# Kernel optimization log

Hardware: AMD Instinct MI355X
Metric: run time of the kernel (lower is better)

## Reference

```python
import jax, jax.numpy as jnp
import numpy as np

B, H, S, D = 2, 16, 2048, 64


def setup_inputs() -> dict:
    key = jax.random.key(0)
    kq, kk, kv = jax.random.split(key, 3)
    q = jax.random.normal(kq, (B, H, S, D), dtype=jnp.float32)
    k = jax.random.normal(kk, (B, H, S, D), dtype=jnp.float32)
    v = jax.random.normal(kv, (B, H, S, D), dtype=jnp.float32)
    # True = attend (lower triangular); positions where mask == False get -1e9
    causal_mask = jnp.tril(jnp.ones((S, S), dtype=bool))
    return {"q": q, "k": k, "v": v, "causal_mask": causal_mask}


def reference(q, k, v, causal_mask):
    scale = q.shape[-1] ** 0.5
    # [b,h,s,d] @ [b,h,d,t] -> [b,h,s,t]
    pre_score = jnp.einsum("bhsd,bhtd->bhst", q, k) / scale
    pre_score = jnp.where(causal_mask, pre_score, jnp.float32(-1e9))
    # SafeSoftmax: stable softmax along last dim
    attn = jax.nn.softmax(pre_score, axis=-1)
    return jnp.einsum("bhst,bhtd->bhsd", attn, v)
```

## Files before the change

### kernel.cpp

```cpp
#include <hip/hip_runtime.h>


typedef __attribute__((ext_vector_type(8))) short short8;
typedef __attribute__((ext_vector_type(4))) short short4v;
typedef __attribute__((ext_vector_type(4))) float floatx4;
typedef __attribute__((ext_vector_type(4))) int intx4;

constexpr int S = 2048;
constexpr int D = 64;
constexpr int KSTR = 72;
constexpr int VSTR = 72;

__device__ inline short f2bf(float x){
    unsigned u = __builtin_bit_cast(unsigned, x);
    unsigned r = u + 0x7FFFu + ((u >> 16) & 1u);
    return (short)(r >> 16);
}
__device__ inline float fast_exp2(float x){ return __builtin_amdgcn_exp2f(x); }

__global__ __launch_bounds__(256, 2)
void fa_fwd_kernel(const float* __restrict__ Q, const float* __restrict__ K,
                   const float* __restrict__ V, float* __restrict__ Out)
{
    __shared__ short sK [2][64 * KSTR];
    __shared__ short sVt[2][64 * VSTR];

    const int tid  = threadIdx.x;
    const int wave = tid >> 6;
    const int lane = tid & 63;
    const int l16  = lane & 15;
    const int quad = lane >> 4;

    const unsigned ub = blockIdx.x;
    const int bh = (int)((ub & 7u) * 4u + (ub >> 7));
    const int qp = (int)((ub >> 3) & 15u);

    const float* Qb = Q + (size_t)bh * S * D;
    const float* Kb = K + (size_t)bh * S * D;
    const float* Vb = V + (size_t)bh * S * D;
    float* Ob = Out + (size_t)bh * S * D;

    const float qscale = 0.125f * 1.44269504f;

    const int kr = tid >> 2;
    const int kc = (tid & 3) * 16;
    const int vd0   = (tid & 15) * 4;
    const int vkey0 = (tid >> 4) * 4;
    const float* kSrc = Kb + (size_t)kr * D + kc;
    const float* vSrc = Vb + (size_t)vkey0 * D + vd0;

    floatx4 kpre[4], vpre[4];
#pragma unroll
    for (int i = 0; i < 4; ++i) kpre[i] = *(const floatx4*)(kSrc + i*4);
#pragma unroll
    for (int r = 0; r < 4; ++r) vpre[r] = *(const floatx4*)(vSrc + (size_t)r*D);

    int pb = 0;
#pragma unroll 1
    for (int seg = 0; seg < 2; ++seg){
        const int qt  = seg ? (31 - qp) : qp;
        const int nkb = qt + 1;
        const int r0  = qt * 64 + wave * 16;

        short8 qa[2];
        {
            const float* qptr = Qb + (size_t)(r0 + l16) * D + quad * 8;
#pragma unroll
            for (int kt = 0; kt < 2; ++kt){
                floatx4 f0 = *(const floatx4*)(qptr + kt*32);
                floatx4 f1 = *(const floatx4*)(qptr + kt*32 + 4);
                short8 v;
                v[0]=f2bf(f0.x*qscale); v[1]=f2bf(f0.y*qscale);
                v[2]=f2bf(f0.z*qscale); v[3]=f2bf(f0.w*qscale);
                v[4]=f2bf(f1.x*qscale); v[5]=f2bf(f1.y*qscale);
                v[6]=f2bf(f1.z*qscale); v[7]=f2bf(f1.w*qscale);
                qa[kt] = v;
            }
        }

        float mrow = -1e30f, lsum = 0.0f;
        floatx4 Oacc[4];
#pragma unroll
        for (int dt = 0; dt < 4; ++dt) Oacc[dt] = (floatx4){0.f,0.f,0.f,0.f};

#pragma unroll 1
        for (int kb = 0; kb < nkb; ++kb){
            const int n0 = kb * 64;

            {
                short8 w0, w1;
                w0[0]=f2bf(kpre[0].x); w0[1]=f2bf(kpre[0].y); w0[2]=f2bf(kpre[0].z); w0[3]=f2bf(kpre[0].w);
                w0[4]=f2bf(kpre[1].x); w0[5]=f2bf(kpre[1].y); w0[6]=f2bf(kpre[1].z); w0[7]=f2bf(kpre[1].w);
                w1[0]=f2bf(kpre[2].x); w1[1]=f2bf(kpre[2].y); w1[2]=f2bf(kpre[2].z); w1[3]=f2bf(kpre[2].w);
                w1[4]=f2bf(kpre[3].x); w1[5]=f2bf(kpre[3].y); w1[6]=f2bf(kpre[3].z); w1[7]=f2bf(kpre[3].w);
                *(short8*)&sK[pb][kr * KSTR + kc]     = w0;
                *(short8*)&sK[pb][kr * KSTR + kc + 8] = w1;
#pragma unroll
                for (int j = 0; j < 4; ++j){
                    short4v sj;
                    sj[0]=f2bf(vpre[0][j]); sj[1]=f2bf(vpre[1][j]);
                    sj[2]=f2bf(vpre[2][j]); sj[3]=f2bf(vpre[3][j]);
                    *(short4v*)&sVt[pb][(vd0 + j) * VSTR + vkey0] = sj;
                }
            }

            {
                const int n0n = (kb + 1 < nkb) ? (n0 + 64) : 0;
                const float* ks = kSrc + (size_t)n0n * D;
                const float* vs = vSrc + (size_t)n0n * D;
#pragma unroll
                for (int i = 0; i < 4; ++i) kpre[i] = *(const floatx4*)(ks + i*4);
#pragma unroll
                for (int r = 0; r < 4; ++r) vpre[r] = *(const floatx4*)(vs + (size_t)r*D);
            }

            __syncthreads();

            const int lastT = min(3, (r0 + 15 - n0) >> 4);

            float p[4][4];
#pragma unroll
            for (int t = 0; t < 4; ++t)
#pragma unroll
                for (int r = 0; r < 4; ++r) p[t][r] = 0.0f;

            float mx = -1e30f;
#pragma unroll
            for (int t = 0; t < 4; ++t){
                if (t > lastT) continue;
                const short8 kf0 = *(const short8*)&sK[pb][(t*16 + l16) * KSTR + quad*8];
                const short8 kf1 = *(const short8*)&sK[pb][(t*16 + l16) * KSTR + 32 + quad*8];
                floatx4 acc = (floatx4){0.f,0.f,0.f,0.f};
                acc = __builtin_amdgcn_mfma_f32_16x16x32_bf16(kf0, qa[0], acc, 0,0,0);
                acc = __builtin_amdgcn_mfma_f32_16x16x32_bf16(kf1, qa[1], acc, 0,0,0);
                if (n0 + t*16 + 15 > r0){
                    const int keyb = n0 + t*16 + quad*4;
                    const int qrow = r0 + l16;
#pragma unroll
                    for (int r = 0; r < 4; ++r)
                        acc[r] = (keyb + r <= qrow) ? acc[r] : -1e9f;
                }
#pragma unroll
                for (int r = 0; r < 4; ++r){ p[t][r] = acc[r]; mx = fmaxf(mx, acc[r]); }
            }
            mx = fmaxf(mx, __shfl_xor(mx, 16, 64));
            mx = fmaxf(mx, __shfl_xor(mx, 32, 64));

            const float mn = fmaxf(mrow, mx);
            const float al = fast_exp2(mrow - mn);
            mrow = mn;

            float rs = 0.0f;
#pragma unroll
            for (int t = 0; t < 4; ++t){
                if (t > lastT) continue;
#pragma unroll
                for (int r = 0; r < 4; ++r){
                    p[t][r] = fast_exp2(p[t][r] - mn);
                    rs += p[t][r];
                }
            }
            rs += __shfl_xor(rs, 16, 64);
            rs += __shfl_xor(rs, 32, 64);
            lsum = lsum * al + rs;
#pragma unroll
            for (int dt = 0; dt < 4; ++dt)
#pragma unroll
                for (int r = 0; r < 4; ++r) Oacc[dt][r] *= al;

            unsigned pk[4][2];
#pragma unroll
            for (int t = 0; t < 4; ++t)
#pragma unroll
                for (int h = 0; h < 2; ++h){
                    unsigned lo = __builtin_bit_cast(unsigned, p[t][2*h]);
                    unsigned hi = __builtin_bit_cast(unsigned, p[t][2*h+1]);
                    pk[t][h] = (lo >> 16) | (hi & 0xFFFF0000u);
                }

            const int addr_lo = (l16 + ((quad & 1) << 5)) << 2;
            const int addr_hi = addr_lo + 64;
            const bool hiQ = quad >= 2;
#pragma unroll
            for (int c = 0; c < 2; ++c){
                if (2*c > lastT) continue;
                const int ta = 2*c, tb = 2*c + 1;
                int a0 = __builtin_amdgcn_ds_bpermute(addr_lo, (int)pk[ta][0]);
                int b0 = __builtin_amdgcn_ds_bpermute(addr_lo, (int)pk[tb][0]);
                int a1 = __builtin_amdgcn_ds_bpermute(addr_lo, (int)pk[ta][1]);
                int b1 = __builtin_amdgcn_ds_bpermute(addr_lo, (int)pk[tb][1]);
                int a2 = __builtin_amdgcn_ds_bpermute(addr_hi, (int)pk[ta][0]);
                int b2 = __builtin_amdgcn_ds_bpermute(addr_hi, (int)pk[tb][0]);
                int a3 = __builtin_amdgcn_ds_bpermute(addr_hi, (int)pk[ta][1]);
                int b3 = __builtin_amdgcn_ds_bpermute(addr_hi, (int)pk[tb][1]);
                union { intx4 i4; short8 s8; } bf;
                bf.i4[0] = hiQ ? b0 : a0;
                bf.i4[1] = hiQ ? b1 : a1;
                bf.i4[2] = hiQ ? b2 : a2;
                bf.i4[3] = hiQ ? b3 : a3;
#pragma unroll
                for (int dt = 0; dt < 4; ++dt){
                    const short8 vf = *(const short8*)&sVt[pb][(dt*16 + l16) * VSTR + c*32 + quad*8];
                    Oacc[dt] = __builtin_amdgcn_mfma_f32_16x16x32_bf16(vf, bf.s8, Oacc[dt], 0,0,0);
                }
            }
            pb ^= 1;
        }

        const float inv = 1.0f / lsum;
        float* op = Ob + (size_t)(r0 + l16) * D + quad * 4;
#pragma unroll
        for (int dt = 0; dt < 4; ++dt){
            floatx4 o;
#pragma unroll
            for (int r = 0; r < 4; ++r) o[r] = Oacc[dt][r] * inv;
            *(floatx4*)(op + dt*16) = o;
        }
    }
}

extern "C" void kernel_launch(void* const* d_in, const int* in_sizes, int n_in,
                              void* d_out, int out_size, void* d_ws, size_t ws_size,
                              hipStream_t stream) {
    const float* q = (const float*)d_in[0];
    const float* k = (const float*)d_in[1];
    const float* v = (const float*)d_in[2];
    float* out = (float*)d_out;
    dim3 grid(512);
    dim3 block(256);
    hipLaunchKernelGGL(fa_fwd_kernel, grid, block, 0, stream, q, k, v, out);
}
```

Measured before the change: 154.6 us.

## Prepack K/V into bf16 MFMA fragment layout in workspace before attention

Adds a prepass kernel that converts K and V to bf16 and stores them in workspace already arranged in MFMA fragment order, with V transposed. The attention kernel then copies these fragments into shared memory with plain vector loads and stores, avoiding per-block conversion and the strided transpose. The grid also changes from 512 blocks each handling a paired light and heavy query tile to 1024 blocks of one tile each, launched heaviest-first, with 4 blocks per CU instead of 2. The cost is an extra kernel launch and a bf16 write and read pass through workspace; the original kernel is kept as a fallback when the workspace is too small.

After: 145.9 us. -5.6%, faster.

```diff
diff --git a/kernel.cpp b/kernel.cpp
--- a/kernel.cpp
+++ b/kernel.cpp
@@ -8,8 +8,9 @@
 
 constexpr int S = 2048;
 constexpr int D = 64;
-constexpr int KSTR = 72;
-constexpr int VSTR = 72;
+constexpr size_t TILE_SH = 8 * 64 * 8;
+constexpr size_t TENSOR_SH = 32ull * 32 * TILE_SH;
+constexpr size_t WS_NEEDED = 2 * TENSOR_SH * 2;
 
 __device__ inline short f2bf(float x){
     unsigned u = __builtin_bit_cast(unsigned, x);
@@ -18,12 +19,49 @@
 }
 __device__ inline float fast_exp2(float x){ return __builtin_amdgcn_exp2f(x); }
 
-__global__ __launch_bounds__(256, 2)
-void fa_fwd_kernel(const float* __restrict__ Q, const float* __restrict__ K,
-                   const float* __restrict__ V, float* __restrict__ Out)
+__global__ __launch_bounds__(256)
+void prepack_kernel(const float* __restrict__ K, const float* __restrict__ V,
+                    short* __restrict__ Kf, short* __restrict__ Vf)
 {
-    __shared__ short sK [2][64 * KSTR];
-    __shared__ short sVt[2][64 * VSTR];
+    const int blk = blockIdx.x;
+    const int bh = blk >> 5, kb = blk & 31;
+    const int tid = threadIdx.x;
+    const float* Kb = K + (size_t)bh * S * D + (size_t)kb * 64 * D;
+    const float* Vb = V + (size_t)bh * S * D + (size_t)kb * 64 * D;
+    short* Kfb = Kf + (size_t)(bh * 32 + kb) * TILE_SH;
+    short* Vfb = Vf + (size_t)(bh * 32 + kb) * TILE_SH;
+#pragma unroll
+    for (int h = 0; h < 2; ++h){
+        const int s = tid + h * 256;
+        const int f = s >> 6, lane = s & 63;
+        const int l16 = lane & 15, quad = lane >> 4;
+        {
+            const int t = f >> 1, kt = f & 1;
+            const float* src = Kb + (size_t)(t*16 + l16) * D + kt*32 + quad*8;
+            floatx4 a = *(const floatx4*)src;
+            floatx4 b = *(const floatx4*)(src + 4);
+            short8 v;
+            v[0]=f2bf(a.x); v[1]=f2bf(a.y); v[2]=f2bf(a.z); v[3]=f2bf(a.w);
+            v[4]=f2bf(b.x); v[5]=f2bf(b.y); v[6]=f2bf(b.z); v[7]=f2bf(b.w);
+            *(short8*)&Kfb[(size_t)s * 8] = v;
+        }
+        {
+            const int c = f >> 2, dt = f & 3;
+            const int d = dt*16 + l16, key0 = c*32 + quad*8;
+            short8 v;
+#pragma unroll
+            for (int j = 0; j < 8; ++j)
+                v[j] = f2bf(Vb[(size_t)(key0 + j) * D + d]);
+            *(short8*)&Vfb[(size_t)s * 8] = v;
+        }
+    }
+}
+
+__global__ __launch_bounds__(256, 4)
+void fa_fwd_kernel(const float* __restrict__ Q, const short* __restrict__ Kf,
+                   const short* __restrict__ Vf, float* __restrict__ Out)
+{
+    __shared__ short sF[2][16 * 512];
 
     const int tid  = threadIdx.x;
     const int wave = tid >> 6;
@@ -32,36 +70,202 @@
     const int quad = lane >> 4;
 
     const unsigned ub = blockIdx.x;
+    const int i  = (int)(ub >> 3);
+    const int bh = (int)(ub & 7u) * 4 + (i & 3);
+    const int qt = 31 - (i >> 2);
+    const int r0 = qt * 64 + wave * 16;
+    const int nkb = qt + 1;
+
+    const float* Qb = Q + (size_t)bh * S * D;
+    const short* Kfb = Kf + (size_t)bh * 32 * TILE_SH;
+    const short* Vfb = Vf + (size_t)bh * 32 * TILE_SH;
+    float* Ob = Out + (size_t)bh * S * D;
+
+    const float qscale = 0.125f * 1.44269504f;
+
+    short8 qa[2];
+    {
+        const float* qptr = Qb + (size_t)(r0 + l16) * D + quad * 8;
+#pragma unroll
+        for (int kt = 0; kt < 2; ++kt){
+            floatx4 f0 = *(const floatx4*)(qptr + kt*32);
+            floatx4 f1 = *(const floatx4*)(qptr + kt*32 + 4);
+            short8 v;
+            v[0]=f2bf(f0.x*qscale); v[1]=f2bf(f0.y*qscale);
+            v[2]=f2bf(f0.z*qscale); v[3]=f2bf(f0.w*qscale);
+            v[4]=f2bf(f1.x*qscale); v[5]=f2bf(f1.y*qscale);
+            v[6]=f2bf(f1.z*qscale); v[7]=f2bf(f1.w*qscale);
+            qa[kt] = v;
+        }
+    }
+
+    float mrow = -1e30f, lsum = 0.0f;
+    floatx4 Oacc[4];
+#pragma unroll
+    for (int dt = 0; dt < 4; ++dt) Oacc[dt] = (floatx4){0.f,0.f,0.f,0.f};
+
+    intx4 pre[4];
+    auto prefetch = [&](int kb){
+#pragma unroll
+        for (int u = 0; u < 4; ++u){
+            const int sl = wave * 4 + u;
+            const short* src = (sl < 8)
+                ? Kfb + (size_t)kb * TILE_SH + (size_t)(sl * 64 + lane) * 8
+                : Vfb + (size_t)kb * TILE_SH + (size_t)((sl - 8) * 64 + lane) * 8;
+            pre[u] = *(const intx4*)src;
+        }
+    };
+
+    prefetch(0);
+    int pb = 0;
+
+#pragma unroll 1
+    for (int kb = 0; kb < nkb; ++kb){
+        const int n0 = kb * 64;
+#pragma unroll
+        for (int u = 0; u < 4; ++u)
+            *(intx4*)&sF[pb][(wave * 4 + u) * 512 + lane * 8] = pre[u];
+        prefetch(kb + 1 < nkb ? kb + 1 : 0);
+        __syncthreads();
+
+        const short* fb = &sF[pb][0];
+        const int lastT = min(3, (r0 + 15 - n0) >> 4);
+
+        float p[4][4];
+        float mx = -1e30f;
+#pragma unroll
+        for (int t = 0; t < 4; ++t){
+#pragma unroll
+            for (int r = 0; r < 4; ++r) p[t][r] = 0.0f;
+            if (t > lastT) continue;
+            const short8 kf0 = *(const short8*)&fb[(t*2    ) * 512 + lane*8];
+            const short8 kf1 = *(const short8*)&fb[(t*2 + 1) * 512 + lane*8];
+            floatx4 acc = (floatx4){0.f,0.f,0.f,0.f};
+            acc = __builtin_amdgcn_mfma_f32_16x16x32_bf16(kf0, qa[0], acc, 0,0,0);
+            acc = __builtin_amdgcn_mfma_f32_16x16x32_bf16(kf1, qa[1], acc, 0,0,0);
+            if (n0 + t*16 + 15 > r0){
+                const int keyb = n0 + t*16 + quad*4;
+                const int qrow = r0 + l16;
+#pragma unroll
+                for (int r = 0; r < 4; ++r)
+                    acc[r] = (keyb + r <= qrow) ? acc[r] : -1e9f;
+            }
+#pragma unroll
+            for (int r = 0; r < 4; ++r){ p[t][r] = acc[r]; mx = fmaxf(mx, acc[r]); }
+        }
+        mx = fmaxf(mx, __shfl_xor(mx, 16, 64));
+        mx = fmaxf(mx, __shfl_xor(mx, 32, 64));
+
+        const float mn = fmaxf(mrow, mx);
+        const float al = fast_exp2(mrow - mn);
+        mrow = mn;
+
+        float rs = 0.0f;
+#pragma unroll
+        for (int t = 0; t < 4; ++t){
+            if (t > lastT) continue;
+#pragma unroll
+            for (int r = 0; r < 4; ++r){
+                p[t][r] = fast_exp2(p[t][r] - mn);
+                rs += p[t][r];
+            }
+        }
+        rs += __shfl_xor(rs, 16, 64);
+        rs += __shfl_xor(rs, 32, 64);
+        lsum = lsum * al + rs;
+#pragma unroll
+        for (int dt = 0; dt < 4; ++dt)
+#pragma unroll
+            for (int r = 0; r < 4; ++r) Oacc[dt][r] *= al;
+
+        unsigned pk[4][2];
+#pragma unroll
+        for (int t = 0; t < 4; ++t)
+#pragma unroll
+            for (int h = 0; h < 2; ++h){
+                unsigned lo = __builtin_bit_cast(unsigned, p[t][2*h]);
+                unsigned hi = __builtin_bit_cast(unsigned, p[t][2*h+1]);
+                pk[t][h] = (lo >> 16) | (hi & 0xFFFF0000u);
+            }
+
+        const int addr_lo = (l16 + ((quad & 1) << 5)) << 2;
+        const int addr_hi = addr_lo + 64;
+        const bool hiQ = quad >= 2;
+#pragma unroll
+        for (int c = 0; c < 2; ++c){
+            if (2*c > lastT) continue;
+            const int ta = 2*c, tb = 2*c + 1;
+            int a0 = __builtin_amdgcn_ds_bpermute(addr_lo, (int)pk[ta][0]);
+            int b0 = __builtin_amdgcn_ds_bpermute(addr_lo, (int)pk[tb][0]);
+            int a1 = __builtin_amdgcn_ds_bpermute(addr_lo, (int)pk[ta][1]);
+            int b1 = __builtin_amdgcn_ds_bpermute(addr_lo, (int)pk[tb][1]);
+            int a2 = __builtin_amdgcn_ds_bpermute(addr_hi, (int)pk[ta][0]);
+            int b2 = __builtin_amdgcn_ds_bpermute(addr_hi, (int)pk[tb][0]);
+            int a3 = __builtin_amdgcn_ds_bpermute(addr_hi, (int)pk[ta][1]);
+            int b3 = __builtin_amdgcn_ds_bpermute(addr_hi, (int)pk[tb][1]);
+            union { intx4 i4; short8 s8; } bf;
+            bf.i4[0] = hiQ ? b0 : a0;
+            bf.i4[1] = hiQ ? b1 : a1;
+            bf.i4[2] = hiQ ? b2 : a2;
+            bf.i4[3] = hiQ ? b3 : a3;
+#pragma unroll
+            for (int dt = 0; dt < 4; ++dt){
+                const short8 vf = *(const short8*)&fb[(8 + c*4 + dt) * 512 + lane*8];
+                Oacc[dt] = __builtin_amdgcn_mfma_f32_16x16x32_bf16(vf, bf.s8, Oacc[dt], 0,0,0);
+            }
+        }
+        pb ^= 1;
+    }
+
+    const float inv = 1.0f / lsum;
+    float* op = Ob + (size_t)(r0 + l16) * D + quad * 4;
+#pragma unroll
+    for (int dt = 0; dt < 4; ++dt){
+        floatx4 o;
+#pragma unroll
+        for (int r = 0; r < 4; ++r) o[r] = Oacc[dt][r] * inv;
+        *(floatx4*)(op + dt*16) = o;
+    }
+}
+
+constexpr int KSTR = 72;
+constexpr int VSTR = 72;
+__global__ __launch_bounds__(256, 2)
+void fa_fwd_fallback(const float* __restrict__ Q, const float* __restrict__ K,
+                     const float* __restrict__ V, float* __restrict__ Out)
+{
+    __shared__ short sK [2][64 * KSTR];
+    __shared__ short sVt[2][64 * VSTR];
+    const int tid  = threadIdx.x;
+    const int wave = tid >> 6;
+    const int lane = tid & 63;
+    const int l16  = lane & 15;
+    const int quad = lane >> 4;
+    const unsigned ub = blockIdx.x;
     const int bh = (int)((ub & 7u) * 4u + (ub >> 7));
     const int qp = (int)((ub >> 3) & 15u);
-
     const float* Qb = Q + (size_t)bh * S * D;
     const float* Kb = K + (size_t)bh * S * D;
     const float* Vb = V + (size_t)bh * S * D;
     float* Ob = Out + (size_t)bh * S * D;
-
     const float qscale = 0.125f * 1.44269504f;
-
     const int kr = tid >> 2;
     const int kc = (tid & 3) * 16;
     const int vd0   = (tid & 15) * 4;
     const int vkey0 = (tid >> 4) * 4;
     const float* kSrc = Kb + (size_t)kr * D + kc;
     const float* vSrc = Vb + (size_t)vkey0 * D + vd0;
-
     floatx4 kpre[4], vpre[4];
 #pragma unroll
     for (int i = 0; i < 4; ++i) kpre[i] = *(const floatx4*)(kSrc + i*4);
 #pragma unroll
     for (int r = 0; r < 4; ++r) vpre[r] = *(const floatx4*)(vSrc + (size_t)r*D);
-
     int pb = 0;
 #pragma unroll 1
     for (int seg = 0; seg < 2; ++seg){
         const int qt  = seg ? (31 - qp) : qp;
         const int nkb = qt + 1;
         const int r0  = qt * 64 + wave * 16;
-
         short8 qa[2];
         {
             const float* qptr = Qb + (size_t)(r0 + l16) * D + quad * 8;
@@ -77,16 +281,13 @@
                 qa[kt] = v;
             }
         }
-
         float mrow = -1e30f, lsum = 0.0f;
         floatx4 Oacc[4];
 #pragma unroll
         for (int dt = 0; dt < 4; ++dt) Oacc[dt] = (floatx4){0.f,0.f,0.f,0.f};
-
 #pragma unroll 1
         for (int kb = 0; kb < nkb; ++kb){
             const int n0 = kb * 64;
-
             {
                 short8 w0, w1;
                 w0[0]=f2bf(kpre[0].x); w0[1]=f2bf(kpre[0].y); w0[2]=f2bf(kpre[0].z); w0[3]=f2bf(kpre[0].w);
@@ -103,7 +304,6 @@
                     *(short4v*)&sVt[pb][(vd0 + j) * VSTR + vkey0] = sj;
                 }
             }
-
             {
                 const int n0n = (kb + 1 < nkb) ? (n0 + 64) : 0;
                 const float* ks = kSrc + (size_t)n0n * D;
@@ -113,20 +313,14 @@
 #pragma unroll
                 for (int r = 0; r < 4; ++r) vpre[r] = *(const floatx4*)(vs + (size_t)r*D);
             }
-
             __syncthreads();
-
             const int lastT = min(3, (r0 + 15 - n0) >> 4);
-
             float p[4][4];
-#pragma unroll
-            for (int t = 0; t < 4; ++t)
+            float mx = -1e30f;
+#pragma unroll
+            for (int t = 0; t < 4; ++t){
 #pragma unroll
                 for (int r = 0; r < 4; ++r) p[t][r] = 0.0f;
-
-            float mx = -1e30f;
-#pragma unroll
-            for (int t = 0; t < 4; ++t){
                 if (t > lastT) continue;
                 const short8 kf0 = *(const short8*)&sK[pb][(t*16 + l16) * KSTR + quad*8];
                 const short8 kf1 = *(const short8*)&sK[pb][(t*16 + l16) * KSTR + 32 + quad*8];
@@ -145,11 +339,9 @@
             }
             mx = fmaxf(mx, __shfl_xor(mx, 16, 64));
             mx = fmaxf(mx, __shfl_xor(mx, 32, 64));
-
             const float mn = fmaxf(mrow, mx);
             const float al = fast_exp2(mrow - mn);
             mrow = mn;
-
             float rs = 0.0f;
 #pragma unroll
             for (int t = 0; t < 4; ++t){
@@ -167,7 +359,6 @@
             for (int dt = 0; dt < 4; ++dt)
 #pragma unroll
                 for (int r = 0; r < 4; ++r) Oacc[dt][r] *= al;
-
             unsigned pk[4][2];
 #pragma unroll
             for (int t = 0; t < 4; ++t)
@@ -177,7 +368,6 @@
                     unsigned hi = __builtin_bit_cast(unsigned, p[t][2*h+1]);
                     pk[t][h] = (lo >> 16) | (hi & 0xFFFF0000u);
                 }
-
             const int addr_lo = (l16 + ((quad & 1) << 5)) << 2;
             const int addr_hi = addr_lo + 64;
             const bool hiQ = quad >= 2;
@@ -206,7 +396,6 @@
             }
             pb ^= 1;
         }
-
         const float inv = 1.0f / lsum;
         float* op = Ob + (size_t)(r0 + l16) * D + quad * 4;
 #pragma unroll
@@ -226,7 +415,12 @@
     const float* k = (const float*)d_in[1];
     const float* v = (const float*)d_in[2];
     float* out = (float*)d_out;
-    dim3 grid(512);
-    dim3 block(256);
-    hipLaunchKernelGGL(fa_fwd_kernel, grid, block, 0, stream, q, k, v, out);
+    if (ws_size >= WS_NEEDED){
+        short* Kf = (short*)d_ws;
+        short* Vf = Kf + TENSOR_SH;
+        hipLaunchKernelGGL(prepack_kernel, dim3(1024), dim3(256), 0, stream, k, v, Kf, Vf);
+        hipLaunchKernelGGL(fa_fwd_kernel, dim3(1024), dim3(256), 0, stream, q, Kf, Vf, out);
+    } else {
+        hipLaunchKernelGGL(fa_fwd_fallback, dim3(512), dim3(256), 0, stream, q, k, v, out);
+    }
 }
```
